# Kernel optimization log

Hardware: AMD Instinct MI355X
Metric: run time of the kernel (lower is better)

Reference implementation:

```python
import jax, jax.numpy as jnp
import numpy as np


def _quantum_act(x, act_w):
    # LearnedQuantumActivation, eval mode (no phase noise): softmax-weighted mix of 9 activations
    w = jax.nn.softmax(act_w)
    mish = x * jnp.tanh(jax.nn.softplus(x))
    return (w[0] * jax.nn.sigmoid(x) + w[1] * jax.nn.elu(x) + w[2] * jnp.tanh(x)
            + w[3] * jax.nn.relu(x) + w[4] * jax.nn.silu(x)
            + w[5] * jax.nn.gelu(x, approximate=False) + w[6] * jax.nn.selu(x)
            + w[7] * mish + w[8] * x)


def setup_inputs() -> dict:
    B, D, U, N = 1024, 1024, 2048, 4      # batch, input_dim, max_units, num_branches
    M, MD, O, H = 2048, 1024, 512, 64     # memory_size, memory_dim, output_dim, critic hidden
    key = jax.random.key(0)
    ks = jax.random.split(key, 16)
    g = lambda k, shape, s=0.02: jax.random.normal(k, shape, dtype=jnp.float32) * s
    return {
        "x": jax.random.normal(ks[0], (B, D), dtype=jnp.float32),
        "w": g(ks[1], (D, U, N)),
        "b": jnp.zeros((U, N), jnp.float32),
        "gate_w": g(ks[2], (D, N)), "gate_b": jnp.zeros((N,), jnp.float32),
        "act_w": jnp.ones((9,), jnp.float32),
        "mask": jnp.ones((U,), jnp.float32),          # neuron_mask, initial_units == max_units
        "mem": g(ks[3], (M, MD), 0.05),
        "att_w": g(ks[4], (U, M)), "att_b": jnp.zeros((M,), jnp.float32),
        "write_w": g(ks[5], (U, MD)), "write_b": jnp.zeros((MD,), jnp.float32),
        "update_gate": jnp.full((M,), 0.5, jnp.float32),
        "out_w": g(ks[6], (U, O)), "out_b": jnp.zeros((O,), jnp.float32),
        "cw1": g(ks[7], (MD, H // 2)), "cb1": jnp.zeros((H // 2,), jnp.float32),
        "cw2": g(ks[8], (O, H // 2)), "cb2": jnp.zeros((H // 2,), jnp.float32),
        "cw3": g(ks[9], (U, H // 2)), "cb3": jnp.zeros((H // 2,), jnp.float32),
        "cw4": g(ks[10], (3 * (H // 2), H)), "cb4": jnp.zeros((H,), jnp.float32),
        "cw5": g(ks[11], (H, 2)), "cb5": jnp.zeros((2,), jnp.float32),
        "meta_threshold": jnp.float32(0.5),
    }


def reference(x, w, b, gate_w, gate_b, act_w, mask, mem, att_w, att_b,
              write_w, write_b, update_gate, out_w, out_b,
              cw1, cb1, cw2, cb2, cw3, cb3, cw4, cb4, cw5, cb5, meta_threshold):
    # Dendritic plastic dense: per-branch projections mixed by a learned softmax branch gate
    pre = jnp.einsum('bi,iun->bun', x, w) + b               # (B, U, N)
    gate = jax.nn.softmax(x @ gate_w + gate_b, axis=-1)     # (B, N)
    hidden = _quantum_act(jnp.einsum('bun,bn->bu', pre, gate), act_w) * mask  # (B, U)
    # Episodic memory read + write (write is returned instead of in-place assign)
    read_att = jax.nn.softmax(hidden @ att_w + att_b, axis=-1)  # (B, M)
    read = read_att @ mem                                       # (B, MD)
    cand = jnp.tanh(hidden @ write_w + write_b)                 # (B, MD)
    u = (jnp.mean(read_att, axis=0) * update_gate)[:, None]     # (M, 1)
    new_mem = mem * (1.0 - u) + u * jnp.mean(cand, axis=0)      # (M, MD)
    # Prediction head
    preds = hidden @ out_w + out_b                              # (B, O)
    # Metacognitive critic gating
    mf = jax.nn.relu(read @ cw1 + cb1)
    pf = jax.nn.relu(preds @ cw2 + cb2)
    hf = jax.nn.relu(hidden @ cw3 + cb3)
    fused = jax.nn.relu(jnp.concatenate([mf, pf, hf], axis=-1) @ cw4 + cb4)
    outs = fused @ cw5 + cb5
    gating = jax.nn.sigmoid(outs[:, 0:1] - meta_threshold)
    return (preds * gating, new_mem)
```

## Files before the change

### kernel.cpp

```cpp
#include <hip/hip_runtime.h>
#include <hip/hip_bf16.h>
#include <math.h>

typedef __attribute__((ext_vector_type(4))) float f32x4;
typedef __attribute__((ext_vector_type(8))) short s16x8;
typedef __attribute__((ext_vector_type(4))) short s16x4;
typedef __hip_bfloat16 bf16;

#define MB (1024ull*1024ull)
#define GATE_OFF    (0ull)
#define ACTW_OFF    (16ull*1024)
#define U_OFF       (20ull*1024)
#define CMEAN_OFF   (28ull*1024)
#define PART_OFF    (64ull*1024)
#define HIDDEN_OFF  (1ull*MB)
#define RATT_OFF    (5ull*MB)
#define CAND_OFF    (9ull*MB)
#define PREDS_OFF   (11ull*MB)
#define READ_OFF    (13ull*MB)
#define XBF_OFF     (17ull*MB)
#define WT_OFF      (19ull*MB)
#define CATT_OFF    (35ull*MB)
#define MEMT_OFF    (49ull*MB)
#define READ2_OFF   WT_OFF

__device__ __forceinline__ short f2bf_s(float f) {
    bf16 h = __float2bfloat16(f);
    return *reinterpret_cast<short*>(&h);
}

__device__ __forceinline__ void async_load16(const bf16* g, short* l) {
    __builtin_amdgcn_global_load_lds((const __attribute__((address_space(1))) void*)g,
                                     (__attribute__((address_space(3))) void*)l, 16, 0, 0);
}

__device__ __forceinline__ float fast_tanh(float x) {
    float e2x = __expf(2.f * x);
    return 1.f - 2.f / (e2x + 1.f);
}

__device__ __forceinline__ float qact(float x, const float* w) {
    float ex  = __expf(x);
    float r1  = 1.f / (1.f + ex);
    float sig = 1.f - r1;
    float em1 = ex - 1.f;
    float elu = x > 0.f ? x : em1;
    float e2x = ex * ex;
    float th  = 1.f - 2.f / (e2x + 1.f);
    float rel = fmaxf(x, 0.f);
    float silu = x * sig;
    float u   = 0.7978845608028654f * (x + 0.044715f * x * x * x);
    float e2u = __expf(2.f * u);
    float gel = x * (1.f - 1.f / (e2u + 1.f));
    float sel = 1.0507009873554805f * (x > 0.f ? x : 1.6732632423543772f * em1);
    float t   = 1.f + ex;
    float t2  = t * t;
    float mish = x * (1.f - 2.f / (t2 + 1.f));
    return w[0]*sig + w[1]*elu + w[2]*th + w[3]*rel + w[4]*silu
         + w[5]*gel + w[6]*sel + w[7]*mish + w[8]*x;
}

__global__ __launch_bounds__(256) void k_transpose(const float* __restrict__ in,
                                                   bf16* __restrict__ out, int R, int C) {
    __shared__ short tile[64][66];
    int k0 = blockIdx.y*64, n0 = blockIdx.x*64;
    int tx = threadIdx.x, ty = threadIdx.y;
    #pragma unroll
    for (int j = 0; j < 16; j++) {
        int k = ty + j*4;
        tile[tx][k] = f2bf_s(in[(size_t)(k0 + k)*C + n0 + tx]);
    }
    __syncthreads();
    int t = ty*64 + tx;
    int kp = t & 31, nrow = t >> 5;
    #pragma unroll
    for (int jj = 0; jj < 8; jj++) {
        int n = nrow + jj*8;
        unsigned lo = (unsigned short)tile[n][kp*2];
        unsigned hi = (unsigned short)tile[n][kp*2 + 1];
        *reinterpret_cast<unsigned*>(&out[(size_t)(n0 + n)*R + k0 + kp*2]) = lo | (hi << 16);
    }
}

__global__ __launch_bounds__(256) void k_cvt(const float* __restrict__ in,
                                             bf16* __restrict__ out) {
    int i = blockIdx.x*256 + threadIdx.x;
    f32x4 v = ((const f32x4*)in)[i];
    s16x4 o;
    #pragma unroll
    for (int j = 0; j < 4; j++) o[j] = f2bf_s(v[j]);
    ((s16x4*)out)[i] = o;
}

__global__ __launch_bounds__(256) void k_gate(const float* __restrict__ x,
                                              const float* __restrict__ gw,
                                              const float* __restrict__ gb,
                                              const float* __restrict__ aw_in,
                                              float* __restrict__ gate,
                                              float* __restrict__ actw) {
    int b = blockIdx.x, t = threadIdx.x, w = t >> 6, lane = t & 63;
    __shared__ float l[4];
    float s = 0.f;
    for (int k = lane; k < 1024; k += 64)
        s += x[(size_t)b*1024 + k] * gw[k*4 + w];
    #pragma unroll
    for (int off = 32; off; off >>= 1) s += __shfl_xor(s, off);
    if (lane == 0) l[w] = s + gb[w];
    __syncthreads();
    if (t == 0) {
        float m = fmaxf(fmaxf(l[0], l[1]), fmaxf(l[2], l[3]));
        float e0 = __expf(l[0]-m), e1 = __expf(l[1]-m), e2 = __expf(l[2]-m), e3 = __expf(l[3]-m);
        float inv = 1.f / (e0+e1+e2+e3);
        gate[b*4+0] = e0*inv; gate[b*4+1] = e1*inv;
        gate[b*4+2] = e2*inv; gate[b*4+3] = e3*inv;
    }
    if (b == 0 && t == 64) {
        float a[9]; float m = -1e30f;
        for (int i = 0; i < 9; i++) { a[i] = aw_in[i]; m = fmaxf(m, a[i]); }
        float ss = 0.f;
        for (int i = 0; i < 9; i++) { a[i] = __expf(a[i]-m); ss += a[i]; }
        float inv = 1.f / ss;
        for (int i = 0; i < 9; i++) actw[i] = a[i]*inv;
    }
}

template <int MODE, int TM>
__global__ __launch_bounds__(256, 2) void gemm_bt(
        const bf16* __restrict__ A, const bf16* __restrict__ Bt,
        int K, int lda, int ldb, int kOffset,
        const float* __restrict__ bias, const float* __restrict__ bias2,
        const float* __restrict__ bias3,
        float* __restrict__ outF, float* __restrict__ outF2,
        bf16* __restrict__ outH, bf16* __restrict__ outH2,
        const float* __restrict__ gate, const float* __restrict__ actw,
        const float* __restrict__ mask, int outStride) {
    constexpr int MI = TM / 32;
    __shared__ __align__(16) union SMem {
        struct { short a[TM*32]; short b[128*32]; } tl;
        float z[TM*32];
    } sm;
    int t = threadIdx.x, lane = t & 63;
    int rowBase = blockIdx.y * TM, colBase = blockIdx.x * 128;
    int lm = lane & 15, lq = lane >> 4;
    int w = t >> 6;
    int qm = (w >> 1) * (TM/2), qn = (w & 1) * 64;

    A  += (size_t)kOffset * blockIdx.z;
    Bt += (size_t)kOffset * blockIdx.z;

    f32x4 acc[MI][4];
    #pragma unroll
    for (int i = 0; i < MI; i++)
        #pragma unroll
        for (int j = 0; j < 4; j++) acc[i][j] = (f32x4){0.f, 0.f, 0.f, 0.f};

    int cb0 = w*128 + lane, cb1 = cb0 + 64;
    int rb0 = cb0 >> 2, kb0 = (cb0 & 3) * 8;
    int rb1 = cb1 >> 2, kb1 = (cb1 & 3) * 8;
    short* dstB0 = sm.tl.b + w*1024;
    short* dstB1 = sm.tl.b + w*1024 + 512;
    int ca0 = (TM == 128) ? (w*128 + lane) : (w*64 + lane);
    int ra0 = ca0 >> 2, ka0 = (ca0 & 3) * 8;
    int ra1 = (ca0 + 64) >> 2, ka1 = ((ca0 + 64) & 3) * 8;
    short* dstA0 = sm.tl.a + ((TM == 128) ? w*1024 : w*512);
    short* dstA1 = sm.tl.a + w*1024 + 512;

    for (int k0 = 0; k0 < K; k0 += 32) {
        __syncthreads();
        async_load16(A + (size_t)(rowBase + ra0)*lda + k0 + ka0, dstA0);
        if (TM == 128)
            async_load16(A + (size_t)(rowBase + ra1)*lda + k0 + ka1, dstA1);
        async_load16(Bt + (size_t)(colBase + rb0)*ldb + k0 + kb0, dstB0);
        async_load16(Bt + (size_t)(colBase + rb1)*ldb + k0 + kb1, dstB1);
        __syncthreads();
        s16x8 af[MI], bfr[4];
        #pragma unroll
        for (int mi = 0; mi < MI; mi++)
            af[mi] = *reinterpret_cast<const s16x8*>(sm.tl.a + (qm + mi*16 + lm)*32 + lq*8);
        #pragma unroll
        for (int ni = 0; ni < 4; ni++)
            bfr[ni] = *reinterpret_cast<const s16x8*>(sm.tl.b + (qn + ni*16 + lm)*32 + lq*8);
        #pragma unroll
        for (int mi = 0; mi < MI; mi++)
            #pragma unroll
            for (int ni = 0; ni < 4; ni++)
                acc[mi][ni] = __builtin_amdgcn_mfma_f32_16x16x32_bf16(af[mi], bfr[ni], acc[mi][ni], 0, 0, 0);
    }

    if (MODE == 4) {
        __syncthreads();
        #pragma unroll
        for (int mi = 0; mi < MI; mi++) {
            int rowl0 = qm + mi*16 + lq*4;
            #pragma unroll
            for (int ni = 0; ni < 4; ni++) {
                int col = colBase + qn + ni*16 + lm;
                int n = col & 3;
                float bb = bias[col];
                f32x4 v = acc[mi][ni];
                #pragma unroll
                for (int r = 0; r < 4; r++) v[r] = (v[r] + bb) * gate[(rowBase + rowl0 + r)*4 + n];
                #pragma unroll
                for (int r = 0; r < 4; r++) v[r] += __shfl_xor(v[r], 1);
                #pragma unroll
                for (int r = 0; r < 4; r++) v[r] += __shfl_xor(v[r], 2);
                if ((lane & 3) == 0) {
                    int ul = ((w & 1) << 4) + ni*4 + (lm >> 2);
                    #pragma unroll
                    for (int r = 0; r < 4; r++)
                        sm.z[(rowl0 + r)*32 + ul] = v[r];
                }
            }
        }
        __syncthreads();
        float aw[9];
        #pragma unroll
        for (int i = 0; i < 9; i++) aw[i] = actw[i];
        int u0 = colBase >> 2;
        #pragma unroll
        for (int i = 0; i < TM/8; i++) {
            int idx = t + i*256;
            int row = idx >> 5, ul = idx & 31;
            int ug = u0 + ul;
            float zz = sm.z[idx];
            outH[(size_t)(rowBase + row)*outStride + ug] = __float2bfloat16(qact(zz, aw) * mask[ug]);
        }
    } else if (MODE == 5) {
        #pragma unroll
        for (int mi = 0; mi < MI; mi++) {
            int row0 = rowBase + qm + mi*16 + lq*4;
            #pragma unroll
            for (int ni = 0; ni < 4; ni++) {
                int col = colBase + qn + ni*16 + lm;
                if (col < 2048) {
                    float bb = bias[col];
                    #pragma unroll
                    for (int r = 0; r < 4; r++)
                        outH[(size_t)(row0 + r)*2048 + col] = __float2bfloat16(acc[mi][ni][r] + bb);
                } else if (col < 3072) {
                    int c = col - 2048;
                    float bb = bias2[c];
                    #pragma unroll
                    for (int r = 0; r < 4; r++)
                        outH2[(size_t)(row0 + r)*1024 + c] = __float2bfloat16(fast_tanh(acc[mi][ni][r] + bb));
                } else {
                    int c = col - 3072;
                    float bb = bias3[c];
                    #pragma unroll
                    for (int r = 0; r < 4; r++)
                        outF[(size_t)(row0 + r)*512 + c] = acc[mi][ni][r] + bb;
                }
            }
        }
    } else {
        float* of = blockIdx.z ? outF2 : outF;
        #pragma unroll
        for (int mi = 0; mi < MI; mi++) {
            int row0 = rowBase + qm + mi*16 + lq*4;
            #pragma unroll
            for (int ni = 0; ni < 4; ni++) {
                int col = colBase + qn + ni*16 + lm;
                #pragma unroll
                for (int r = 0; r < 4; r++)
                    of[(size_t)(row0 + r)*outStride + col] = acc[mi][ni][r];
            }
        }
    }
}

__global__ __launch_bounds__(256) void k_softmax(bf16* __restrict__ ratt) {
    int b = blockIdx.x, t = threadIdx.x, w = t >> 6, lane = t & 63;
    __shared__ float red[8];
    bf16* row = ratt + (size_t)b*2048;
    float v[8];
    float mx = -1e30f;
    #pragma unroll
    for (int j = 0; j < 8; j++) {
        v[j] = __bfloat162float(row[t + j*256]);
        mx = fmaxf(mx, v[j]);
    }
    #pragma unroll
    for (int off = 32; off; off >>= 1) mx = fmaxf(mx, __shfl_xor(mx, off));
    if (lane == 0) red[w] = mx;
    __syncthreads();
    mx = fmaxf(fmaxf(red[0], red[1]), fmaxf(red[2], red[3]));
    float s = 0.f;
    #pragma unroll
    for (int j = 0; j < 8; j++) { v[j] = __expf(v[j] - mx); s += v[j]; }
    #pragma unroll
    for (int off = 32; off; off >>= 1) s += __shfl_xor(s, off);
    if (lane == 0) red[4 + w] = s;
    __syncthreads();
    float inv = 1.f / (red[4] + red[5] + red[6] + red[7]);
    #pragma unroll
    for (int j = 0; j < 8; j++)
        row[t + j*256] = __float2bfloat16(v[j] * inv);
}

__global__ __launch_bounds__(256) void k_colpart(const bf16* __restrict__ ratt,
                                                 const bf16* __restrict__ cand,
                                                 float* __restrict__ part) {
    int ct = blockIdx.x, rc = blockIdx.y, t = threadIdx.x;
    int col = ct*256 + t;
    const bf16* src; int stride, c;
    if (ct < 8) { src = ratt; stride = 2048; c = col; }
    else        { src = cand; stride = 1024; c = col - 2048; }
    float s = 0.f;
    int r0 = rc*128;
    for (int r = 0; r < 128; r++)
        s += __bfloat162float(src[(size_t)(r0 + r)*stride + c]);
    part[rc*3072 + col] = s;
}

__global__ __launch_bounds__(256) void k_colfin(const float* __restrict__ part,
                                                const float* __restrict__ update_gate,
                                                float* __restrict__ u,
                                                float* __restrict__ cmean) {
    int col = blockIdx.x*256 + threadIdx.x;
    float s = 0.f;
    #pragma unroll
    for (int rc = 0; rc < 8; rc++) s += part[rc*3072 + col];
    s *= (1.f/1024.f);
    if (col < 2048) u[col] = s * update_gate[col];
    else            cmean[col - 2048] = s;
}

__global__ __launch_bounds__(256) void k_newmem(const float* __restrict__ mem,
                                                const float* __restrict__ u,
                                                const float* __restrict__ cmean,
                                                float* __restrict__ out1) {
    int idx = blockIdx.x*256 + threadIdx.x;
    int m = idx >> 10, d = idx & 1023;
    float um = u[m];
    out1[idx] = mem[idx] * (1.f - um) + um * cmean[d];
}

__global__ __launch_bounds__(256) void k_critic(
        const float* __restrict__ readv, const float* __restrict__ readv2,
        const float* __restrict__ preds, const bf16* __restrict__ hidden,
        const float* cw1, const float* cb1, const float* cw2, const float* cb2,
        const float* cw3, const float* cb3, const float* cw4, const float* cb4,
        const float* cw5, const float* cb5, const float* thr,
        float* __restrict__ out0) {
    __shared__ __align__(16) float sx[2*1024];
    __shared__ __align__(16) float sp[2*512];
    __shared__ __align__(16) short sh[2*2048];
    __shared__ __align__(16) f32x4 part[2][32][8];
    __shared__ float feat[2][96];
    __shared__ float fused[2][64];
    __shared__ float gsh[2];
    int b0 = blockIdx.x * 2, t = threadIdx.x;
    int j4 = t & 7, kg = t >> 3;

    ((f32x4*)sx)[t]       = ((const f32x4*)(readv + (size_t)b0*1024))[t]
                          + ((const f32x4*)(readv2 + (size_t)b0*1024))[t];
    ((f32x4*)sx)[t + 256] = ((const f32x4*)(readv + (size_t)b0*1024))[t + 256]
                          + ((const f32x4*)(readv2 + (size_t)b0*1024))[t + 256];
    ((f32x4*)sp)[t]       = ((const f32x4*)(preds + (size_t)b0*512))[t];
    ((s16x8*)sh)[t]       = ((const s16x8*)(hidden + (size_t)b0*2048))[t];
    ((s16x8*)sh)[t + 256] = ((const s16x8*)(hidden + (size_t)b0*2048))[t + 256];
    __syncthreads();

    {
        const f32x4* wv = (const f32x4*)cw1;
        f32x4 a0 = (f32x4){0,0,0,0}, a1 = (f32x4){0,0,0,0};
        int k0 = kg*32;
        #pragma unroll 4
        for (int k = k0; k < k0 + 32; k++) {
            f32x4 wq = wv[k*8 + j4];
            a0 += sx[k] * wq;
            a1 += sx[1024 + k] * wq;
        }
        part[0][kg][j4] = a0; part[1][kg][j4] = a1;
    }
    __syncthreads();
    if (t < 64) {
        int r = t >> 5, f = t & 31;
        float s = 0.f;
        #pragma unroll
        for (int i = 0; i < 32; i++) s += part[r][i][f >> 2][f & 3];
        feat[r][f] = fmaxf(s + cb1[f], 0.f);
    }
    __syncthreads();
    {
        const f32x4* wv = (const f32x4*)cw2;
        f32x4 a0 = (f32x4){0,0,0,0}, a1 = (f32x4){0,0,0,0};
        int k0 = kg*16;
        #pragma unroll 4
        for (int k = k0; k < k0 + 16; k++) {
            f32x4 wq = wv[k*8 + j4];
            a0 += sp[k] * wq;
            a1 += sp[512 + k] * wq;
        }
        part[0][kg][j4] = a0; part[1][kg][j4] = a1;
    }
    __syncthreads();
    if (t < 64) {
        int r = t >> 5, f = t & 31;
        float s = 0.f;
        #pragma unroll
        for (int i = 0; i < 32; i++) s += part[r][i][f >> 2][f & 3];
        feat[r][32 + f] = fmaxf(s + cb2[f], 0.f);
    }
    __syncthreads();
    {
        const f32x4* wv = (const f32x4*)cw3;
        f32x4 a0 = (f32x4){0,0,0,0}, a1 = (f32x4){0,0,0,0};
        int k0 = kg*64;
        #pragma unroll 4
        for (int k = k0; k < k0 + 64; k++) {
            f32x4 wq = wv[k*8 + j4];
            float h0 = __bfloat162float(*reinterpret_cast<const bf16*>(&sh[k]));
            float h1 = __bfloat162float(*reinterpret_cast<const bf16*>(&sh[2048 + k]));
            a0 += h0 * wq;
            a1 += h1 * wq;
        }
        part[0][kg][j4] = a0; part[1][kg][j4] = a1;
    }
    __syncthreads();
    if (t < 64) {
        int r = t >> 5, f = t & 31;
        float s = 0.f;
        #pragma unroll
        for (int i = 0; i < 32; i++) s += part[r][i][f >> 2][f & 3];
        feat[r][64 + f] = fmaxf(s + cb3[f], 0.f);
    }
    __syncthreads();
    if (t < 128) {
        int r = t >> 6, uu = t & 63;
        float s = 0.f;
        #pragma unroll 8
        for (int k = 0; k < 96; k++) s += feat[r][k] * cw4[k*64 + uu];
        fused[r][uu] = fmaxf(s + cb4[uu], 0.f);
    }
    __syncthreads();
    if (t < 128) {
        int r = t >> 6, lane = t & 63;
        float v = fused[r][lane] * cw5[lane*2];
        #pragma unroll
        for (int off = 32; off; off >>= 1) v += __shfl_xor(v, off);
        if (lane == 0)
            gsh[r] = 1.f / (1.f + __expf(-(v + cb5[0] - thr[0])));
    }
    __syncthreads();
    #pragma unroll
    for (int idx = t; idx < 1024; idx += 256) {
        int r = idx >> 9, o = idx & 511;
        out0[(size_t)(b0 + r)*512 + o] = sp[r*512 + o] * gsh[r];
    }
}

extern "C" void kernel_launch(void* const* d_in, const int* in_sizes, int n_in,
                              void* d_out, int out_size, void* d_ws, size_t ws_size,
                              hipStream_t stream) {
    const float* x        = (const float*)d_in[0];
    const float* w_       = (const float*)d_in[1];
    const float* b_bias   = (const float*)d_in[2];
    const float* gate_w   = (const float*)d_in[3];
    const float* gate_b   = (const float*)d_in[4];
    const float* act_w    = (const float*)d_in[5];
    const float* mask     = (const float*)d_in[6];
    const float* mem      = (const float*)d_in[7];
    const float* att_w    = (const float*)d_in[8];
    const float* att_b    = (const float*)d_in[9];
    const float* write_w  = (const float*)d_in[10];
    const float* write_b  = (const float*)d_in[11];
    const float* upd_gate = (const float*)d_in[12];
    const float* out_w    = (const float*)d_in[13];
    const float* out_b    = (const float*)d_in[14];
    const float* cw1 = (const float*)d_in[15]; const float* cb1 = (const float*)d_in[16];
    const float* cw2 = (const float*)d_in[17]; const float* cb2 = (const float*)d_in[18];
    const float* cw3 = (const float*)d_in[19]; const float* cb3 = (const float*)d_in[20];
    const float* cw4 = (const float*)d_in[21]; const float* cb4 = (const float*)d_in[22];
    const float* cw5 = (const float*)d_in[23]; const float* cb5 = (const float*)d_in[24];
    const float* thr = (const float*)d_in[25];

    char* ws = (char*)d_ws;
    float* gate   = (float*)(ws + GATE_OFF);
    float* actw   = (float*)(ws + ACTW_OFF);
    float* uvec   = (float*)(ws + U_OFF);
    float* cmean  = (float*)(ws + CMEAN_OFF);
    float* part   = (float*)(ws + PART_OFF);
    bf16*  hidden = (bf16*)(ws + HIDDEN_OFF);
    bf16*  ratt   = (bf16*)(ws + RATT_OFF);
    bf16*  cand   = (bf16*)(ws + CAND_OFF);
    float* preds  = (float*)(ws + PREDS_OFF);
    float* readv  = (float*)(ws + READ_OFF);
    float* readv2 = (float*)(ws + READ2_OFF);
    bf16*  xbf    = (bf16*)(ws + XBF_OFF);
    bf16*  wT     = (bf16*)(ws + WT_OFF);
    bf16*  catT   = (bf16*)(ws + CATT_OFF);
    bf16*  memT   = (bf16*)(ws + MEMT_OFF);

    float* out0 = (float*)d_out;
    float* out1 = out0 + 1024*512;

    dim3 tb(64, 4);
    k_cvt<<<1024, 256, 0, stream>>>(x, xbf);
    k_transpose<<<dim3(128, 16), tb, 0, stream>>>(w_,      wT,                  1024, 8192);
    k_transpose<<<dim3(32, 32),  tb, 0, stream>>>(att_w,   catT,                2048, 2048);
    k_transpose<<<dim3(16, 32),  tb, 0, stream>>>(write_w, catT + 2048ull*2048, 2048, 1024);
    k_transpose<<<dim3(8, 32),   tb, 0, stream>>>(out_w,   catT + 3072ull*2048, 2048, 512);
    k_transpose<<<dim3(16, 32),  tb, 0, stream>>>(mem,     memT,                2048, 1024);

    k_gate<<<1024, 256, 0, stream>>>(x, gate_w, gate_b, act_w, gate, actw);

    gemm_bt<4, 64><<<dim3(64, 16), 256, 0, stream>>>(xbf, wT, 1024, 1024, 1024, 0,
        b_bias, nullptr, nullptr, nullptr, nullptr, hidden, nullptr, gate, actw, mask, 2048);
    gemm_bt<5, 64><<<dim3(28, 16), 256, 0, stream>>>(hidden, catT, 2048, 2048, 2048, 0,
        att_b, write_b, out_b, preds, nullptr, ratt, cand, nullptr, nullptr, nullptr, 0);
    k_softmax<<<1024, 256, 0, stream>>>(ratt);
    gemm_bt<3, 64><<<dim3(8, 16, 2), 256, 0, stream>>>(ratt, memT, 1024, 2048, 2048, 1024,
        nullptr, nullptr, nullptr, readv, readv2, nullptr, nullptr, nullptr, nullptr, nullptr, 1024);

    k_colpart<<<dim3(12, 8), 256, 0, stream>>>(ratt, cand, part);
    k_colfin<<<12, 256, 0, stream>>>(part, upd_gate, uvec, cmean);
    k_newmem<<<8192, 256, 0, stream>>>(mem, uvec, cmean, out1);
    k_critic<<<512, 256, 0, stream>>>(readv, readv2, preds, hidden,
        cw1, cb1, cw2, cb2, cw3, cb3, cw4, cb4, cw5, cb5, thr, out0);
}
```

Baseline: 303.8 us.

## Double-buffer GEMM LDS tiles and merge preprocessing kernels into one launch

The bf16 GEMM now keeps two LDS tile buffers and issues the async global-to-LDS loads for the next K-slice before running MFMAs on the current one. This removes one barrier per iteration and is meant to overlap load latency with compute. Separately, the x conversion, gate softmax, activation-weight softmax and five weight transposes are folded into a single 6400-block kernel that branches on block index, which removes several launch gaps. The cost is doubled LDS use per GEMM block, which could lower occupancy, and a heterogeneous prepass kernel whose blocks do uneven work.

After: 273.1 us, median of 2. 10.1% less time.

```diff
diff --git a/kernel.cpp b/kernel.cpp
--- a/kernel.cpp
+++ b/kernel.cpp
@@ -60,18 +60,18 @@
          + w[5]*gel + w[6]*sel + w[7]*mish + w[8]*x;
 }
 
-__global__ __launch_bounds__(256) void k_transpose(const float* __restrict__ in,
-                                                   bf16* __restrict__ out, int R, int C) {
+__device__ __forceinline__ void do_transpose(const float* __restrict__ in,
+                                             bf16* __restrict__ out, int R, int C,
+                                             int bx, int by, int t) {
     __shared__ short tile[64][66];
-    int k0 = blockIdx.y*64, n0 = blockIdx.x*64;
-    int tx = threadIdx.x, ty = threadIdx.y;
+    int k0 = by*64, n0 = bx*64;
+    int tx = t & 63, ty = t >> 6;
     #pragma unroll
     for (int j = 0; j < 16; j++) {
         int k = ty + j*4;
         tile[tx][k] = f2bf_s(in[(size_t)(k0 + k)*C + n0 + tx]);
     }
     __syncthreads();
-    int t = ty*64 + tx;
     int kp = t & 31, nrow = t >> 5;
     #pragma unroll
     for (int jj = 0; jj < 8; jj++) {
@@ -82,45 +82,63 @@
     }
 }
 
-__global__ __launch_bounds__(256) void k_cvt(const float* __restrict__ in,
-                                             bf16* __restrict__ out) {
-    int i = blockIdx.x*256 + threadIdx.x;
-    f32x4 v = ((const f32x4*)in)[i];
-    s16x4 o;
-    #pragma unroll
-    for (int j = 0; j < 4; j++) o[j] = f2bf_s(v[j]);
-    ((s16x4*)out)[i] = o;
-}
-
-__global__ __launch_bounds__(256) void k_gate(const float* __restrict__ x,
-                                              const float* __restrict__ gw,
-                                              const float* __restrict__ gb,
-                                              const float* __restrict__ aw_in,
-                                              float* __restrict__ gate,
-                                              float* __restrict__ actw) {
-    int b = blockIdx.x, t = threadIdx.x, w = t >> 6, lane = t & 63;
-    __shared__ float l[4];
-    float s = 0.f;
-    for (int k = lane; k < 1024; k += 64)
-        s += x[(size_t)b*1024 + k] * gw[k*4 + w];
-    #pragma unroll
-    for (int off = 32; off; off >>= 1) s += __shfl_xor(s, off);
-    if (lane == 0) l[w] = s + gb[w];
-    __syncthreads();
-    if (t == 0) {
-        float m = fmaxf(fmaxf(l[0], l[1]), fmaxf(l[2], l[3]));
-        float e0 = __expf(l[0]-m), e1 = __expf(l[1]-m), e2 = __expf(l[2]-m), e3 = __expf(l[3]-m);
-        float inv = 1.f / (e0+e1+e2+e3);
-        gate[b*4+0] = e0*inv; gate[b*4+1] = e1*inv;
-        gate[b*4+2] = e2*inv; gate[b*4+3] = e3*inv;
-    }
-    if (b == 0 && t == 64) {
-        float a[9]; float m = -1e30f;
-        for (int i = 0; i < 9; i++) { a[i] = aw_in[i]; m = fmaxf(m, a[i]); }
-        float ss = 0.f;
-        for (int i = 0; i < 9; i++) { a[i] = __expf(a[i]-m); ss += a[i]; }
-        float inv = 1.f / ss;
-        for (int i = 0; i < 9; i++) actw[i] = a[i]*inv;
+__global__ __launch_bounds__(256) void k_prepass(
+        const float* __restrict__ x, bf16* __restrict__ xbf,
+        const float* __restrict__ gw, const float* __restrict__ gb,
+        const float* __restrict__ aw_in,
+        float* __restrict__ gate, float* __restrict__ actw,
+        const float* __restrict__ w_, bf16* __restrict__ wT,
+        const float* __restrict__ att_w, const float* __restrict__ write_w,
+        const float* __restrict__ out_w, bf16* __restrict__ catT,
+        const float* __restrict__ mem, bf16* __restrict__ memT) {
+    int blk = blockIdx.x, t = threadIdx.x;
+    if (blk < 1024) {
+        int i = blk*256 + t;
+        f32x4 v = ((const f32x4*)x)[i];
+        s16x4 o;
+        #pragma unroll
+        for (int j = 0; j < 4; j++) o[j] = f2bf_s(v[j]);
+        ((s16x4*)xbf)[i] = o;
+        if (blk == 0 && t == 64) {
+            float a[9]; float m = -1e30f;
+            for (int i2 = 0; i2 < 9; i2++) { a[i2] = aw_in[i2]; m = fmaxf(m, a[i2]); }
+            float ss = 0.f;
+            for (int i2 = 0; i2 < 9; i2++) { a[i2] = __expf(a[i2]-m); ss += a[i2]; }
+            float inv = 1.f / ss;
+            for (int i2 = 0; i2 < 9; i2++) actw[i2] = a[i2]*inv;
+        }
+    } else if (blk < 2048) {
+        int b = blk - 1024, w = t >> 6, lane = t & 63;
+        __shared__ float l[4];
+        float s = 0.f;
+        for (int k = lane; k < 1024; k += 64)
+            s += x[(size_t)b*1024 + k] * gw[k*4 + w];
+        #pragma unroll
+        for (int off = 32; off; off >>= 1) s += __shfl_xor(s, off);
+        if (lane == 0) l[w] = s + gb[w];
+        __syncthreads();
+        if (t == 0) {
+            float m = fmaxf(fmaxf(l[0], l[1]), fmaxf(l[2], l[3]));
+            float e0 = __expf(l[0]-m), e1 = __expf(l[1]-m), e2 = __expf(l[2]-m), e3 = __expf(l[3]-m);
+            float inv = 1.f / (e0+e1+e2+e3);
+            gate[b*4+0] = e0*inv; gate[b*4+1] = e1*inv;
+            gate[b*4+2] = e2*inv; gate[b*4+3] = e3*inv;
+        }
+    } else if (blk < 4096) {
+        int rel = blk - 2048;
+        do_transpose(w_, wT, 1024, 8192, rel & 127, rel >> 7, t);
+    } else if (blk < 5120) {
+        int rel = blk - 4096;
+        do_transpose(att_w, catT, 2048, 2048, rel & 31, rel >> 5, t);
+    } else if (blk < 5632) {
+        int rel = blk - 5120;
+        do_transpose(write_w, catT + 2048ull*2048, 2048, 1024, rel & 15, rel >> 4, t);
+    } else if (blk < 5888) {
+        int rel = blk - 5632;
+        do_transpose(out_w, catT + 3072ull*2048, 2048, 512, rel & 7, rel >> 3, t);
+    } else {
+        int rel = blk - 5888;
+        do_transpose(mem, memT, 2048, 1024, rel & 15, rel >> 4, t);
     }
 }
 
@@ -136,7 +154,7 @@
         const float* __restrict__ mask, int outStride) {
     constexpr int MI = TM / 32;
     __shared__ __align__(16) union SMem {
-        struct { short a[TM*32]; short b[128*32]; } tl;
+        struct { short a[2][TM*32]; short b[2][128*32]; } tl;
         float z[TM*32];
     } sm;
     int t = threadIdx.x, lane = t & 63;
@@ -157,34 +175,41 @@
     int cb0 = w*128 + lane, cb1 = cb0 + 64;
     int rb0 = cb0 >> 2, kb0 = (cb0 & 3) * 8;
     int rb1 = cb1 >> 2, kb1 = (cb1 & 3) * 8;
-    short* dstB0 = sm.tl.b + w*1024;
-    short* dstB1 = sm.tl.b + w*1024 + 512;
     int ca0 = (TM == 128) ? (w*128 + lane) : (w*64 + lane);
     int ra0 = ca0 >> 2, ka0 = (ca0 & 3) * 8;
     int ra1 = (ca0 + 64) >> 2, ka1 = ((ca0 + 64) & 3) * 8;
-    short* dstA0 = sm.tl.a + ((TM == 128) ? w*1024 : w*512);
-    short* dstA1 = sm.tl.a + w*1024 + 512;
-
+
+    auto issueLoads = [&](int k0, int ib) {
+        short* bA = sm.tl.a[ib];
+        short* bB = sm.tl.b[ib];
+        async_load16(A + (size_t)(rowBase + ra0)*lda + k0 + ka0,
+                     bA + ((TM == 128) ? w*1024 : w*512));
+        if (TM == 128)
+            async_load16(A + (size_t)(rowBase + ra1)*lda + k0 + ka1, bA + w*1024 + 512);
+        async_load16(Bt + (size_t)(colBase + rb0)*ldb + k0 + kb0, bB + w*1024);
+        async_load16(Bt + (size_t)(colBase + rb1)*ldb + k0 + kb1, bB + w*1024 + 512);
+    };
+
+    issueLoads(0, 0);
+    int ib = 0;
     for (int k0 = 0; k0 < K; k0 += 32) {
         __syncthreads();
-        async_load16(A + (size_t)(rowBase + ra0)*lda + k0 + ka0, dstA0);
-        if (TM == 128)
-            async_load16(A + (size_t)(rowBase + ra1)*lda + k0 + ka1, dstA1);
-        async_load16(Bt + (size_t)(colBase + rb0)*ldb + k0 + kb0, dstB0);
-        async_load16(Bt + (size_t)(colBase + rb1)*ldb + k0 + kb1, dstB1);
-        __syncthreads();
+        if (k0 + 32 < K) issueLoads(k0 + 32, ib ^ 1);
+        const short* cA = sm.tl.a[ib];
+        const short* cB = sm.tl.b[ib];
         s16x8 af[MI], bfr[4];
         #pragma unroll
         for (int mi = 0; mi < MI; mi++)
-            af[mi] = *reinterpret_cast<const s16x8*>(sm.tl.a + (qm + mi*16 + lm)*32 + lq*8);
+            af[mi] = *reinterpret_cast<const s16x8*>(cA + (qm + mi*16 + lm)*32 + lq*8);
         #pragma unroll
         for (int ni = 0; ni < 4; ni++)
-            bfr[ni] = *reinterpret_cast<const s16x8*>(sm.tl.b + (qn + ni*16 + lm)*32 + lq*8);
+            bfr[ni] = *reinterpret_cast<const s16x8*>(cB + (qn + ni*16 + lm)*32 + lq*8);
         #pragma unroll
         for (int mi = 0; mi < MI; mi++)
             #pragma unroll
             for (int ni = 0; ni < 4; ni++)
                 acc[mi][ni] = __builtin_amdgcn_mfma_f32_16x16x32_bf16(af[mi], bfr[ni], acc[mi][ni], 0, 0, 0);
+        ib ^= 1;
     }
 
     if (MODE == 4) {
@@ -495,15 +520,8 @@
     float* out0 = (float*)d_out;
     float* out1 = out0 + 1024*512;
 
-    dim3 tb(64, 4);
-    k_cvt<<<1024, 256, 0, stream>>>(x, xbf);
-    k_transpose<<<dim3(128, 16), tb, 0, stream>>>(w_,      wT,                  1024, 8192);
-    k_transpose<<<dim3(32, 32),  tb, 0, stream>>>(att_w,   catT,                2048, 2048);
-    k_transpose<<<dim3(16, 32),  tb, 0, stream>>>(write_w, catT + 2048ull*2048, 2048, 1024);
-    k_transpose<<<dim3(8, 32),   tb, 0, stream>>>(out_w,   catT + 3072ull*2048, 2048, 512);
-    k_transpose<<<dim3(16, 32),  tb, 0, stream>>>(mem,     memT,                2048, 1024);
-
-    k_gate<<<1024, 256, 0, stream>>>(x, gate_w, gate_b, act_w, gate, actw);
+    k_prepass<<<6400, 256, 0, stream>>>(x, xbf, gate_w, gate_b, act_w, gate, actw,
+        w_, wT, att_w, write_w, out_w, catT, mem, memT);
 
     gemm_bt<4, 64><<<dim3(64, 16), 256, 0, stream>>>(xbf, wT, 1024, 1024, 1024, 0,
         b_bias, nullptr, nullptr, nullptr, nullptr, hidden, nullptr, gate, actw, mask, 2048);
```
